# Kernel optimization log

Hardware: AMD Instinct MI355X
Metric: run time of the kernel (lower is better)

## Reference

```python
import math
import jax, jax.numpy as jnp
import numpy as np

EPS = 1e-12
INV_4PI = 1.0 / (4.0 * math.pi)
B, NF = 32768, 3
RES_THETA, RES_PHI = 21, 41


def _make_quadrature(res_theta, res_phi):
    theta = np.linspace(0.0, math.pi, res_theta, dtype=np.float32)
    phi = np.linspace(0.0, 2.0 * math.pi, res_phi, dtype=np.float32)
    tm = 0.5 * (theta[:-1] + theta[1:])
    pm = 0.5 * (phi[:-1] + phi[1:])
    dth = theta[1:] - theta[:-1]
    dph = phi[1:] - phi[:-1]
    st, ct = np.sin(tm), np.cos(tm)
    sp, cp = np.sin(pm), np.cos(pm)
    vx = np.outer(st, cp).reshape(-1)
    vy = np.outer(st, sp).reshape(-1)
    vz = np.outer(ct, np.ones_like(pm)).reshape(-1)
    w = np.outer(st * dth, dph).reshape(-1)
    return (jnp.asarray(vx), jnp.asarray(vy), jnp.asarray(vz), jnp.asarray(w))


def setup_inputs() -> dict:
    key = jax.random.key(0)
    k1, k2, k3 = jax.random.split(key, 3)
    # positive densities O(1), flux magnitude <= 0.9*N (physically valid moments)
    dens = jax.random.uniform(k1, (B, 2, NF), minval=0.3, maxval=1.0, dtype=jnp.float32)
    fdir = jax.random.normal(k2, (B, 2, NF, 3), dtype=jnp.float32)
    fdir = fdir / jnp.clip(jnp.linalg.norm(fdir, axis=-1, keepdims=True), 1e-6)
    fmag = jax.random.uniform(k3, (B, 2, NF), minval=0.0, maxval=0.9, dtype=jnp.float32)
    F = fdir * (dens * fmag)[..., None]
    F4_in = jnp.concatenate([F, dens[..., None]], axis=-1)  # [B,2,NF,4]
    dir_x, dir_y, dir_z, quad_w = _make_quadrature(RES_THETA, RES_PHI)
    return {"F4_in": F4_in, "dir_x": dir_x, "dir_y": dir_y, "dir_z": dir_z, "quad_w": quad_w}


def _z_approxbis(f):
    f = jnp.clip(f, 0.0, 0.999999)
    f2 = f * f
    f4 = f2 * f2
    f6 = f4 * f2
    f8 = f4 * f4
    denom = 3.0 - 1.00651 * f2 - 0.962251 * f4 + 1.47353 * f6 - 0.48953 * f8
    p = 1.0 - 2.0 * (1.0 - f) * (1.0 + 1.01524 * f) / jnp.clip(denom, EPS)
    return 2.0 * f / jnp.clip(1.0 - p, 1e-06)


def _z_over_sinh_z(z):
    small = jnp.abs(z) < 1e-4
    zs = jnp.where(small, 1.0, z)  # avoid 0/0 in unused branch
    series = 1.0 - z * z / 6.0 + (z * z) * (z * z) / 120.0
    return jnp.where(small, series, zs / jnp.sinh(zs))


def _forward(F4_in, dir_x, dir_y, dir_z, quad_w):
    nf = F4_in.shape[2]
    N_e, N_ebar = F4_in[:, 0, 0, 3], F4_in[:, 1, 0, 3]
    F_e, F_ebar = F4_in[:, 0, 0, :3], F4_in[:, 1, 0, :3]
    if nf > 1:
        N_x = jnp.mean(F4_in[:, 0, 1:, 3], axis=1)
        N_xbar = jnp.mean(F4_in[:, 1, 1:, 3], axis=1)
        F_x = jnp.mean(F4_in[:, 0, 1:, :3], axis=1)
        F_xbar = jnp.mean(F4_in[:, 1, 1:, :3], axis=1)
    else:
        N_x, N_xbar, F_x, F_xbar = N_e, N_ebar, F_e, F_ebar
    N = jnp.clip(jnp.stack([N_e, N_ebar, N_x, N_xbar], axis=1), EPS)  # [B,4]
    F = jnp.stack([F_e, F_ebar, F_x, F_xbar], axis=1)  # [B,4,3]
    normF = jnp.sqrt(jnp.sum(F * F, axis=2))  # [B,4]
    fluxfac = jnp.clip(normF / N, 0.0, 0.999999)
    Z = _z_approxbis(fluxfac)  # [B,4]
    # mu: projection of unit direction onto flux direction, [B,4,D]
    mu = (F[:, :, 0, None] * dir_x + F[:, :, 1, None] * dir_y + F[:, :, 2, None] * dir_z) / jnp.clip(normF[..., None], EPS)
    g = N[..., None] * INV_4PI * _z_over_sinh_z(Z)[..., None] * jnp.exp(Z[..., None] * mu)  # [B,4,D]
    gnue, gnuebar, gnux, gnuxbar = g[:, 0], g[:, 1], g[:, 2], g[:, 3]
    delta = gnue - gnuebar - gnux + gnuxbar  # [B,D]
    Hpos = (delta >= 0.0).astype(g.dtype)
    Hneg = 1.0 - Hpos
    Iplus = jnp.sum(quad_w * jnp.maximum(delta, 0.0), axis=1)  # [B]
    Iminus = jnp.sum(quad_w * jnp.maximum(-delta, 0.0), axis=1)
    Ip_s = jnp.clip(Iplus, EPS)
    Im_s = jnp.clip(Iminus, EPS)
    third = jnp.full_like(Iplus, 1.0 / 3.0)
    coeff_pos = jnp.clip(jnp.where(Iplus < Iminus, third, 1.0 - 2.0 / 3.0 * (Im_s / Ip_s)), 0.0, 1.0)
    coeff_neg = jnp.clip(jnp.where(Iplus < Iminus, 1.0 - 2.0 / 3.0 * (Ip_s / Im_s), third), 0.0, 1.0)
    Psur = coeff_pos[:, None] * Hpos + coeff_neg[:, None] * Hneg  # [B,D]
    gnue_t = gnue * Psur + gnux * (1.0 - Psur)
    gnuebar_t = gnuebar * Psur + gnuxbar * (1.0 - Psur)
    gnux_t = 0.5 * (1.0 - Psur) * gnue + 0.5 * (1.0 + Psur) * gnux
    gnuxbar_t = 0.5 * (1.0 - Psur) * gnuebar + 0.5 * (1.0 + Psur) * gnuxbar
    g_t = jnp.stack([gnue_t, gnuebar_t, gnux_t, gnuxbar_t], axis=1)  # [B,4,D]
    gw = g_t * quad_w  # [B,4,D]
    newN = jnp.sum(gw, axis=2)  # [B,4]
    newF = jnp.stack([jnp.sum(gw * dir_x, axis=2), jnp.sum(gw * dir_y, axis=2), jnp.sum(gw * dir_z, axis=2)], axis=2)  # [B,4,3]
    b = F4_in.shape[0]
    if nf > 1:
        F_nu = jnp.concatenate([newF[:, 0:1], jnp.broadcast_to(newF[:, 2:3], (b, nf - 1, 3))], axis=1)
        F_nubar = jnp.concatenate([newF[:, 1:2], jnp.broadcast_to(newF[:, 3:4], (b, nf - 1, 3))], axis=1)
        N_nu = jnp.concatenate([newN[:, 0:1], jnp.broadcast_to(newN[:, 2:3], (b, nf - 1))], axis=1)
        N_nubar = jnp.concatenate([newN[:, 1:2], jnp.broadcast_to(newN[:, 3:4], (b, nf - 1))], axis=1)
    else:
        F_nu, F_nubar = newF[:, 0:1], newF[:, 1:2]
        N_nu, N_nubar = newN[:, 0:1], newN[:, 1:2]
    nu = jnp.concatenate([F_nu, N_nu[..., None]], axis=-1)  # [B,NF,4]
    nubar = jnp.concatenate([F_nubar, N_nubar[..., None]], axis=-1)
    F4mix = jnp.stack([nu, nubar], axis=1)  # [B,2,NF,4]
    growth = jnp.sqrt(jnp.clip(Iplus * Iminus, 0.0))
    return (F4mix, growth)


def reference(F4_in, dir_x, dir_y, dir_z, quad_w):
    return _forward(F4_in, dir_x, dir_y, dir_z, quad_w)
```

## Files before the change

kernel.cpp:

```cpp
#include <hip/hip_runtime.h>
#include <math.h>

#define EPSF     1e-12f
#define INV_4PI  0.07957747154594767f
#define LOG2E    1.4426950408889634f

typedef float v2f __attribute__((ext_vector_type(2)));

#if __has_builtin(__builtin_elementwise_fma)
#define FMA2(a, b, c) __builtin_elementwise_fma((a), (b), (c))
#else
#define FMA2(a, b, c) ((a) * (b) + (c))
#endif

#define EXP2(x) __builtin_amdgcn_exp2f(x)

__device__ __forceinline__ float zapprox(float f) {
    float f2 = f * f;
    float f4 = f2 * f2;
    float f6 = f4 * f2;
    float f8 = f4 * f4;
    float denom = 3.0f - 1.00651f * f2 - 0.962251f * f4 + 1.47353f * f6 - 0.48953f * f8;
    denom = fmaxf(denom, EPSF);
    float p = 1.0f - 2.0f * (1.0f - f) * (1.0f + 1.01524f * f) / denom;
    return 2.0f * f / fmaxf(1.0f - p, 1e-6f);
}

__device__ __forceinline__ float z_over_sinh(float z) {
    float zz = z * z;
    float series = 1.0f - zz / 6.0f + zz * zz / 120.0f;
    float E = __expf(z);
    float s = 0.5f * (E - 1.0f / E);
    float r = z / s;
    return (z < 1e-4f) ? series : r;
}

__device__ __forceinline__ float4 setup_spec(float N, float Fx, float Fy, float Fz) {
    N = fmaxf(N, EPSF);
    float nf = sqrtf(Fx * Fx + Fy * Fy + Fz * Fz);
    float f  = fminf(fmaxf(nf / N, 0.0f), 0.999999f);
    float Z  = zapprox(f);
    float A  = N * INV_4PI * z_over_sinh(Z);
    float sc = Z * LOG2E / fmaxf(nf, EPSF);
    return make_float4(Fx * sc, Fy * sc, Fz * sc, log2f(A));
}

__global__ __launch_bounds__(256) void spec_kernel(
    const float* __restrict__ F4, float4* __restrict__ ws, int B)
{
    int t = blockIdx.x * blockDim.x + threadIdx.x;
    if (t >= 4 * B) return;
    int b = t >> 2, s = t & 3;
    const float4* row = (const float4*)(F4 + (size_t)b * 24);
    float N, Fx, Fy, Fz;
    if (s == 0) {
        float4 a = row[0];  N = a.w; Fx = a.x; Fy = a.y; Fz = a.z;
    } else if (s == 1) {
        float4 a = row[3];  N = a.w; Fx = a.x; Fy = a.y; Fz = a.z;
    } else if (s == 2) {
        float4 a = row[1], c = row[2];
        N = 0.5f * (a.w + c.w); Fx = 0.5f * (a.x + c.x);
        Fy = 0.5f * (a.y + c.y); Fz = 0.5f * (a.z + c.z);
    } else {
        float4 a = row[4], c = row[5];
        N = 0.5f * (a.w + c.w); Fx = 0.5f * (a.x + c.x);
        Fy = 0.5f * (a.y + c.y); Fz = 0.5f * (a.z + c.z);
    }
    ws[(size_t)b * 4 + s] = setup_spec(N, Fx, Fy, Fz);
}

__device__ __forceinline__ v2f bcast(float x) { v2f r; r.x = x; r.y = x; return r; }

__global__ __launch_bounds__(256, 4) void box3d_kernel(
    const float4* __restrict__ ws,
    const float* __restrict__ dxp, const float* __restrict__ dyp,
    const float* __restrict__ dzp, const float* __restrict__ qwp,
    float* __restrict__ out, int B, int ndir)
{
    __shared__ float4 sAB[400], sCD[400];
    const int npair = ndir >> 1;
    for (int p = threadIdx.x; p < npair; p += blockDim.x) {
        int d0 = 2 * p;
        sAB[p] = make_float4(dxp[d0], dxp[d0 + 1], dyp[d0], dyp[d0 + 1]);
        sCD[p] = make_float4(dzp[d0], dzp[d0 + 1], qwp[d0], qwp[d0 + 1]);
    }
    __syncthreads();

    const int sub = threadIdx.x & 15;
    const int b = blockIdx.x * 16 + (threadIdx.x >> 4);
    if (b >= B) return;

    const float4* wsb = ws + (size_t)b * 4;
    float4 f0 = wsb[0], f1 = wsb[1], f2 = wsb[2], f3 = wsb[3];
    v2f zx0 = bcast(f0.x), zy0 = bcast(f0.y), zz0 = bcast(f0.z), la0 = bcast(f0.w);
    v2f zx1 = bcast(f1.x), zy1 = bcast(f1.y), zz1 = bcast(f1.z), la1 = bcast(f1.w);
    v2f zx2 = bcast(f2.x), zy2 = bcast(f2.y), zz2 = bcast(f2.z), la2 = bcast(f2.w);
    v2f zx3 = bcast(f3.x), zy3 = bcast(f3.y), zz3 = bcast(f3.z), la3 = bcast(f3.w);

    const v2f zero = bcast(0.0f);
    v2f aut0 = zero, aut1 = zero, aut2 = zero, aut3 = zero;
    v2f aup0 = zero, aup1 = zero, aup2 = zero, aup3 = zero;
    v2f avt0 = zero, avt1 = zero, avt2 = zero, avt3 = zero;
    v2f avp0 = zero, avp1 = zero, avp2 = zero, avp3 = zero;
    v2f agx0 = zero, agx1 = zero, agx2 = zero, agx3 = zero;
    v2f agy0 = zero, agy1 = zero, agy2 = zero, agy3 = zero;

    #pragma clang loop unroll(disable)
    for (int p = sub; p < npair; p += 16) {
        float4 ab = sAB[p];
        float4 cd = sCD[p];
        v2f qx; qx.x = ab.x; qx.y = ab.y;
        v2f qy; qy.x = ab.z; qy.y = ab.w;
        v2f qz; qz.x = cd.x; qz.y = cd.y;
        v2f qw; qw.x = cd.z; qw.y = cd.w;

        v2f t0 = FMA2(zx0, qx, FMA2(zy0, qy, FMA2(zz0, qz, la0)));
        v2f t1 = FMA2(zx1, qx, FMA2(zy1, qy, FMA2(zz1, qz, la1)));
        v2f t2 = FMA2(zx2, qx, FMA2(zy2, qy, FMA2(zz2, qz, la2)));
        v2f t3 = FMA2(zx3, qx, FMA2(zy3, qy, FMA2(zz3, qz, la3)));
        v2f g0, g1, g2, g3;
        g0.x = EXP2(t0.x); g0.y = EXP2(t0.y);
        g1.x = EXP2(t1.x); g1.y = EXP2(t1.y);
        g2.x = EXP2(t2.x); g2.y = EXP2(t2.y);
        g3.x = EXP2(t3.x); g3.y = EXP2(t3.y);

        v2f u = g0 - g2, v = g1 - g3;
        v2f wu = qw * u, wv = qw * v;
        v2f wup, wvp;
        wup.x = (u.x >= v.x) ? wu.x : 0.0f;
        wup.y = (u.y >= v.y) ? wu.y : 0.0f;
        wvp.x = (u.x >= v.x) ? wv.x : 0.0f;
        wvp.y = (u.y >= v.y) ? wv.y : 0.0f;
        v2f w2 = qw * g2, w3 = qw * g3;

        aut0 += wu;  aup0 += wup;  avt0 += wv;  avp0 += wvp;  agx0 += w2;  agy0 += w3;
        aut1 = FMA2(wu, qx, aut1);  aup1 = FMA2(wup, qx, aup1);
        avt1 = FMA2(wv, qx, avt1);  avp1 = FMA2(wvp, qx, avp1);
        agx1 = FMA2(w2, qx, agx1);  agy1 = FMA2(w3, qx, agy1);
        aut2 = FMA2(wu, qy, aut2);  aup2 = FMA2(wup, qy, aup2);
        avt2 = FMA2(wv, qy, avt2);  avp2 = FMA2(wvp, qy, avp2);
        agx2 = FMA2(w2, qy, agx2);  agy2 = FMA2(w3, qy, agy2);
        aut3 = FMA2(wu, qz, aut3);  aup3 = FMA2(wup, qz, aup3);
        avt3 = FMA2(wv, qz, avt3);  avp3 = FMA2(wvp, qz, avp3);
        agx3 = FMA2(w2, qz, agx3);  agy3 = FMA2(w3, qz, agy3);
    }

    float ut0 = aut0.x + aut0.y, ut1 = aut1.x + aut1.y, ut2 = aut2.x + aut2.y, ut3 = aut3.x + aut3.y;
    float up0 = aup0.x + aup0.y, up1 = aup1.x + aup1.y, up2 = aup2.x + aup2.y, up3 = aup3.x + aup3.y;
    float vt0 = avt0.x + avt0.y, vt1 = avt1.x + avt1.y, vt2 = avt2.x + avt2.y, vt3 = avt3.x + avt3.y;
    float vp0 = avp0.x + avp0.y, vp1 = avp1.x + avp1.y, vp2 = avp2.x + avp2.y, vp3 = avp3.x + avp3.y;
    float gx0 = agx0.x + agx0.y, gx1 = agx1.x + agx1.y, gx2 = agx2.x + agx2.y, gx3 = agx3.x + agx3.y;
    float gy0 = agy0.x + agy0.y, gy1 = agy1.x + agy1.y, gy2 = agy2.x + agy2.y, gy3 = agy3.x + agy3.y;

    #pragma unroll
    for (int msk = 1; msk <= 8; msk <<= 1) {
        ut0 += __shfl_xor(ut0, msk);  ut1 += __shfl_xor(ut1, msk);
        ut2 += __shfl_xor(ut2, msk);  ut3 += __shfl_xor(ut3, msk);
        up0 += __shfl_xor(up0, msk);  up1 += __shfl_xor(up1, msk);
        up2 += __shfl_xor(up2, msk);  up3 += __shfl_xor(up3, msk);
        vt0 += __shfl_xor(vt0, msk);  vt1 += __shfl_xor(vt1, msk);
        vt2 += __shfl_xor(vt2, msk);  vt3 += __shfl_xor(vt3, msk);
        vp0 += __shfl_xor(vp0, msk);  vp1 += __shfl_xor(vp1, msk);
        vp2 += __shfl_xor(vp2, msk);  vp3 += __shfl_xor(vp3, msk);
        gx0 += __shfl_xor(gx0, msk);  gx1 += __shfl_xor(gx1, msk);
        gx2 += __shfl_xor(gx2, msk);  gx3 += __shfl_xor(gx3, msk);
        gy0 += __shfl_xor(gy0, msk);  gy1 += __shfl_xor(gy1, msk);
        gy2 += __shfl_xor(gy2, msk);  gy3 += __shfl_xor(gy3, msk);
    }

    float ip = fmaxf(up0 - vp0, 0.0f);
    float im = fmaxf(ip - ut0 + vt0, 0.0f);

    float Ips = fmaxf(ip, EPSF), Ims = fmaxf(im, EPSF);
    const float third = 1.0f / 3.0f;
    float cp, cn;
    if (ip < im) {
        cp = third;
        cn = fminf(fmaxf(1.0f - (2.0f / 3.0f) * (Ips / Ims), 0.0f), 1.0f);
    } else {
        cp = fminf(fmaxf(1.0f - (2.0f / 3.0f) * (Ims / Ips), 0.0f), 1.0f);
        cn = third;
    }

    float P0 = cp * up0 + cn * (ut0 - up0), Q0 = cp * vp0 + cn * (vt0 - vp0);
    float P1 = cp * up1 + cn * (ut1 - up1), Q1 = cp * vp1 + cn * (vt1 - vp1);
    float P2 = cp * up2 + cn * (ut2 - up2), Q2 = cp * vp2 + cn * (vt2 - vp2);
    float P3 = cp * up3 + cn * (ut3 - up3), Q3 = cp * vp3 + cn * (vt3 - vp3);

    float4* o4 = (float4*)out + (size_t)b * 6;
    if (sub == 0) {
        o4[0] = make_float4(gx1 + P1, gx2 + P2, gx3 + P3, gx0 + P0);
    } else if (sub == 1) {
        o4[1] = make_float4(gx1 + 0.5f * (ut1 - P1), gx2 + 0.5f * (ut2 - P2),
                            gx3 + 0.5f * (ut3 - P3), gx0 + 0.5f * (ut0 - P0));
    } else if (sub == 2) {
        o4[2] = make_float4(gx1 + 0.5f * (ut1 - P1), gx2 + 0.5f * (ut2 - P2),
                            gx3 + 0.5f * (ut3 - P3), gx0 + 0.5f * (ut0 - P0));
    } else if (sub == 3) {
        o4[3] = make_float4(gy1 + Q1, gy2 + Q2, gy3 + Q3, gy0 + Q0);
    } else if (sub == 4) {
        o4[4] = make_float4(gy1 + 0.5f * (vt1 - Q1), gy2 + 0.5f * (vt2 - Q2),
                            gy3 + 0.5f * (vt3 - Q3), gy0 + 0.5f * (vt0 - Q0));
    } else if (sub == 5) {
        o4[5] = make_float4(gy1 + 0.5f * (vt1 - Q1), gy2 + 0.5f * (vt2 - Q2),
                            gy3 + 0.5f * (vt3 - Q3), gy0 + 0.5f * (vt0 - Q0));
    } else if (sub == 6) {
        out[(size_t)B * 24 + b] = sqrtf(fmaxf(ip * im, 0.0f));
    }
}

extern "C" void kernel_launch(void* const* d_in, const int* in_sizes, int n_in,
                              void* d_out, int out_size, void* d_ws, size_t ws_size,
                              hipStream_t stream) {
    const float* F4 = (const float*)d_in[0];
    const float* dx = (const float*)d_in[1];
    const float* dy = (const float*)d_in[2];
    const float* dz = (const float*)d_in[3];
    const float* qw = (const float*)d_in[4];
    float* out = (float*)d_out;

    int B = in_sizes[0] / 24;
    int ndir = in_sizes[1];
    float4* ws = (float4*)d_ws;

    int t1 = 4 * B;
    spec_kernel<<<(t1 + 255) / 256, 256, 0, stream>>>(F4, ws, B);
    int blocks = (B + 15) / 16;
    box3d_kernel<<<blocks, 256, 0, stream>>>(ws, dx, dy, dz, qw, out, B, ndir);
}
```

Baseline: 96.80 us.

## Exploit antipodal quadrature symmetry and fold weights into exponent

Processes only half of the quadrature directions and derives each mirror direction's exponent as 2*(lambda+log2 w) - t. Sums and differences of the paired values then feed the moment accumulators directly. The quadrature weight is folded into the exponent as log2(w), and the hardware exp2 is replaced by a packed polynomial with ldexp. The thread mapping moves to 8 lanes per batch element and 32 elements per block. This relies on the direction grid being antipodally symmetric with mirror points in the second half, and adds polynomial ALU cost in place of the transcendental unit.

Result: slower. 99.27 us (+2.6%).

```diff
diff --git a/kernel.cpp b/kernel.cpp
--- a/kernel.cpp
+++ b/kernel.cpp
@@ -13,7 +13,22 @@
 #define FMA2(a, b, c) ((a) * (b) + (c))
 #endif
 
-#define EXP2(x) __builtin_amdgcn_exp2f(x)
+__device__ __forceinline__ v2f bcast(float x) { v2f r; r.x = x; r.y = x; return r; }
+
+__device__ __forceinline__ v2f exp2p(v2f x) {
+    v2f n; n.x = __builtin_rintf(x.x); n.y = __builtin_rintf(x.y);
+    v2f r = x - n;
+    const v2f c1 = bcast(0.69314718056f);
+    const v2f c2 = bcast(0.24022650700f);
+    const v2f c3 = bcast(0.05550410866f);
+    const v2f c4 = bcast(0.00961812911f);
+    const v2f c5 = bcast(0.00133335581f);
+    v2f p = FMA2(FMA2(FMA2(FMA2(FMA2(c5, r, c4), r, c3), r, c2), r, c1), r, bcast(1.0f));
+    v2f o;
+    o.x = ldexpf(p.x, (int)n.x);
+    o.y = ldexpf(p.y, (int)n.y);
+    return o;
+}
 
 __device__ __forceinline__ float zapprox(float f) {
     float f2 = f * f;
@@ -69,25 +84,23 @@
     ws[(size_t)b * 4 + s] = setup_spec(N, Fx, Fy, Fz);
 }
 
-__device__ __forceinline__ v2f bcast(float x) { v2f r; r.x = x; r.y = x; return r; }
-
 __global__ __launch_bounds__(256, 4) void box3d_kernel(
     const float4* __restrict__ ws,
     const float* __restrict__ dxp, const float* __restrict__ dyp,
     const float* __restrict__ dzp, const float* __restrict__ qwp,
     float* __restrict__ out, int B, int ndir)
 {
-    __shared__ float4 sAB[400], sCD[400];
-    const int npair = ndir >> 1;
-    for (int p = threadIdx.x; p < npair; p += blockDim.x) {
-        int d0 = 2 * p;
-        sAB[p] = make_float4(dxp[d0], dxp[d0 + 1], dyp[d0], dyp[d0 + 1]);
-        sCD[p] = make_float4(dzp[d0], dzp[d0 + 1], qwp[d0], qwp[d0 + 1]);
+    __shared__ float4 sAB[200], sCD[200];
+    const int npp = ndir >> 2;
+    for (int m = threadIdx.x; m < npp; m += blockDim.x) {
+        int d0 = 2 * m, d1 = d0 + 1;
+        sAB[m] = make_float4(dxp[d0], dxp[d1], dyp[d0], dyp[d1]);
+        sCD[m] = make_float4(dzp[d0], dzp[d1], __log2f(qwp[d0]), __log2f(qwp[d1]));
     }
     __syncthreads();
 
-    const int sub = threadIdx.x & 15;
-    const int b = blockIdx.x * 16 + (threadIdx.x >> 4);
+    const int sub = threadIdx.x & 7;
+    const int b = blockIdx.x * 32 + (threadIdx.x >> 3);
     if (b >= B) return;
 
     const float4* wsb = ws + (size_t)b * 4;
@@ -98,6 +111,7 @@
     v2f zx3 = bcast(f3.x), zy3 = bcast(f3.y), zz3 = bcast(f3.z), la3 = bcast(f3.w);
 
     const v2f zero = bcast(0.0f);
+    const v2f two  = bcast(2.0f);
     v2f aut0 = zero, aut1 = zero, aut2 = zero, aut3 = zero;
     v2f aup0 = zero, aup1 = zero, aup2 = zero, aup3 = zero;
     v2f avt0 = zero, avt1 = zero, avt2 = zero, avt3 = zero;
@@ -106,43 +120,49 @@
     v2f agy0 = zero, agy1 = zero, agy2 = zero, agy3 = zero;
 
     #pragma clang loop unroll(disable)
-    for (int p = sub; p < npair; p += 16) {
-        float4 ab = sAB[p];
-        float4 cd = sCD[p];
+    for (int m = sub; m < npp; m += 8) {
+        float4 ab = sAB[m];
+        float4 cd = sCD[m];
         v2f qx; qx.x = ab.x; qx.y = ab.y;
         v2f qy; qy.x = ab.z; qy.y = ab.w;
         v2f qz; qz.x = cd.x; qz.y = cd.y;
-        v2f qw; qw.x = cd.z; qw.y = cd.w;
-
-        v2f t0 = FMA2(zx0, qx, FMA2(zy0, qy, FMA2(zz0, qz, la0)));
-        v2f t1 = FMA2(zx1, qx, FMA2(zy1, qy, FMA2(zz1, qz, la1)));
-        v2f t2 = FMA2(zx2, qx, FMA2(zy2, qy, FMA2(zz2, qz, la2)));
-        v2f t3 = FMA2(zx3, qx, FMA2(zy3, qy, FMA2(zz3, qz, la3)));
-        v2f g0, g1, g2, g3;
-        g0.x = EXP2(t0.x); g0.y = EXP2(t0.y);
-        g1.x = EXP2(t1.x); g1.y = EXP2(t1.y);
-        g2.x = EXP2(t2.x); g2.y = EXP2(t2.y);
-        g3.x = EXP2(t3.x); g3.y = EXP2(t3.y);
-
-        v2f u = g0 - g2, v = g1 - g3;
-        v2f wu = qw * u, wv = qw * v;
-        v2f wup, wvp;
-        wup.x = (u.x >= v.x) ? wu.x : 0.0f;
-        wup.y = (u.y >= v.y) ? wu.y : 0.0f;
-        wvp.x = (u.x >= v.x) ? wv.x : 0.0f;
-        wvp.y = (u.y >= v.y) ? wv.y : 0.0f;
-        v2f w2 = qw * g2, w3 = qw * g3;
-
-        aut0 += wu;  aup0 += wup;  avt0 += wv;  avp0 += wvp;  agx0 += w2;  agy0 += w3;
-        aut1 = FMA2(wu, qx, aut1);  aup1 = FMA2(wup, qx, aup1);
-        avt1 = FMA2(wv, qx, avt1);  avp1 = FMA2(wvp, qx, avp1);
-        agx1 = FMA2(w2, qx, agx1);  agy1 = FMA2(w3, qx, agy1);
-        aut2 = FMA2(wu, qy, aut2);  aup2 = FMA2(wup, qy, aup2);
-        avt2 = FMA2(wv, qy, avt2);  avp2 = FMA2(wvp, qy, avp2);
-        agx2 = FMA2(w2, qy, agx2);  agy2 = FMA2(w3, qy, agy2);
-        aut3 = FMA2(wu, qz, aut3);  aup3 = FMA2(wup, qz, aup3);
-        avt3 = FMA2(wv, qz, avt3);  avp3 = FMA2(wvp, qz, avp3);
-        agx3 = FMA2(w2, qz, agx3);  agy3 = FMA2(w3, qz, agy3);
+        v2f lw; lw.x = cd.z; lw.y = cd.w;
+
+        v2f b0 = la0 + lw, b1 = la1 + lw, b2 = la2 + lw, b3 = la3 + lw;
+        v2f t0 = FMA2(zx0, qx, FMA2(zy0, qy, FMA2(zz0, qz, b0)));
+        v2f t1 = FMA2(zx1, qx, FMA2(zy1, qy, FMA2(zz1, qz, b1)));
+        v2f t2 = FMA2(zx2, qx, FMA2(zy2, qy, FMA2(zz2, qz, b2)));
+        v2f t3 = FMA2(zx3, qx, FMA2(zy3, qy, FMA2(zz3, qz, b3)));
+        v2f n0 = FMA2(two, b0, -t0);
+        v2f n1 = FMA2(two, b1, -t1);
+        v2f n2 = FMA2(two, b2, -t2);
+        v2f n3 = FMA2(two, b3, -t3);
+
+        v2f gp0 = exp2p(t0), gp1 = exp2p(t1), gp2 = exp2p(t2), gp3 = exp2p(t3);
+        v2f gn0 = exp2p(n0), gn1 = exp2p(n1), gn2 = exp2p(n2), gn3 = exp2p(n3);
+
+        v2f uP = gp0 - gp2, vP = gp1 - gp3;
+        v2f uN = gn0 - gn2, vN = gn1 - gn3;
+
+        v2f suP, svP, suN, svN;
+        suP.x = (uP.x >= vP.x) ? uP.x : 0.0f;  suP.y = (uP.y >= vP.y) ? uP.y : 0.0f;
+        svP.x = (uP.x >= vP.x) ? vP.x : 0.0f;  svP.y = (uP.y >= vP.y) ? vP.y : 0.0f;
+        suN.x = (uN.x >= vN.x) ? uN.x : 0.0f;  suN.y = (uN.y >= vN.y) ? uN.y : 0.0f;
+        svN.x = (uN.x >= vN.x) ? vN.x : 0.0f;  svN.y = (uN.y >= vN.y) ? vN.y : 0.0f;
+
+        v2f s, d;
+        s = uP + uN;   d = uP - uN;
+        aut0 += s; aut1 = FMA2(d, qx, aut1); aut2 = FMA2(d, qy, aut2); aut3 = FMA2(d, qz, aut3);
+        s = suP + suN; d = suP - suN;
+        aup0 += s; aup1 = FMA2(d, qx, aup1); aup2 = FMA2(d, qy, aup2); aup3 = FMA2(d, qz, aup3);
+        s = vP + vN;   d = vP - vN;
+        avt0 += s; avt1 = FMA2(d, qx, avt1); avt2 = FMA2(d, qy, avt2); avt3 = FMA2(d, qz, avt3);
+        s = svP + svN; d = svP - svN;
+        avp0 += s; avp1 = FMA2(d, qx, avp1); avp2 = FMA2(d, qy, avp2); avp3 = FMA2(d, qz, avp3);
+        s = gp2 + gn2; d = gp2 - gn2;
+        agx0 += s; agx1 = FMA2(d, qx, agx1); agx2 = FMA2(d, qy, agx2); agx3 = FMA2(d, qz, agx3);
+        s = gp3 + gn3; d = gp3 - gn3;
+        agy0 += s; agy1 = FMA2(d, qx, agy1); agy2 = FMA2(d, qy, agy2); agy3 = FMA2(d, qz, agy3);
     }
 
     float ut0 = aut0.x + aut0.y, ut1 = aut1.x + aut1.y, ut2 = aut2.x + aut2.y, ut3 = aut3.x + aut3.y;
@@ -153,7 +173,7 @@
     float gy0 = agy0.x + agy0.y, gy1 = agy1.x + agy1.y, gy2 = agy2.x + agy2.y, gy3 = agy3.x + agy3.y;
 
     #pragma unroll
-    for (int msk = 1; msk <= 8; msk <<= 1) {
+    for (int msk = 1; msk <= 4; msk <<= 1) {
         ut0 += __shfl_xor(ut0, msk);  ut1 += __shfl_xor(ut1, msk);
         ut2 += __shfl_xor(ut2, msk);  ut3 += __shfl_xor(ut3, msk);
         up0 += __shfl_xor(up0, msk);  up1 += __shfl_xor(up1, msk);
@@ -225,6 +245,6 @@
 
     int t1 = 4 * B;
     spec_kernel<<<(t1 + 255) / 256, 256, 0, stream>>>(F4, ws, B);
-    int blocks = (B + 15) / 16;
+    int blocks = (B + 31) / 32;
     box3d_kernel<<<blocks, 256, 0, stream>>>(ws, dx, dy, dz, qw, out, B, ndir);
 }
```

## Exploit antipodal quadrature symmetry and restructure box3d as lane-per-batch with LDS reduction

Applied to the files above, without the earlier changes.

Each lane now owns one batch element, and the 16 waves of a 1024-thread block split the first half of the directions. For each direction the kernel also evaluates the antipodal direction by reusing the exponent algebraically (2*lambda - t) and negating the direction in the moment accumulation. This halves direction loads and dot-product work and turns direction reads into wave-uniform loads. The per-batch cross-lane shuffle reduction is replaced by a two-stage LDS reduction across waves, and all six outputs are written by one lane. It relies on the quadrature being antipodally symmetric with equal weights, which holds for this construction but is not checked. It also adds several block-wide barriers and uses a large block.

Result: faster. 92.06 us (-4.9%).

```diff
diff --git a/kernel.cpp b/kernel.cpp
--- a/kernel.cpp
+++ b/kernel.cpp
@@ -14,6 +14,8 @@
 #endif
 
 #define EXP2(x) __builtin_amdgcn_exp2f(x)
+
+__device__ __forceinline__ v2f bcast(float x) { v2f r; r.x = x; r.y = x; return r; }
 
 __device__ __forceinline__ float zapprox(float f) {
     float f2 = f * f;
@@ -69,104 +71,147 @@
     ws[(size_t)b * 4 + s] = setup_spec(N, Fx, Fy, Fz);
 }
 
-__device__ __forceinline__ v2f bcast(float x) { v2f r; r.x = x; r.y = x; return r; }
-
-__global__ __launch_bounds__(256, 4) void box3d_kernel(
+__device__ __forceinline__ void add4(float4& a, const float4 b) {
+    a.x += b.x; a.y += b.y; a.z += b.z; a.w += b.w;
+}
+
+__global__ __launch_bounds__(1024, 8) void box3d_kernel(
     const float4* __restrict__ ws,
     const float* __restrict__ dxp, const float* __restrict__ dyp,
     const float* __restrict__ dzp, const float* __restrict__ qwp,
     float* __restrict__ out, int B, int ndir)
 {
-    __shared__ float4 sAB[400], sCD[400];
-    const int npair = ndir >> 1;
-    for (int p = threadIdx.x; p < npair; p += blockDim.x) {
-        int d0 = 2 * p;
-        sAB[p] = make_float4(dxp[d0], dxp[d0 + 1], dyp[d0], dyp[d0 + 1]);
-        sCD[p] = make_float4(dzp[d0], dzp[d0 + 1], qwp[d0], qwp[d0 + 1]);
-    }
-    __syncthreads();
-
-    const int sub = threadIdx.x & 15;
-    const int b = blockIdx.x * 16 + (threadIdx.x >> 4);
-    if (b >= B) return;
-
-    const float4* wsb = ws + (size_t)b * 4;
-    float4 f0 = wsb[0], f1 = wsb[1], f2 = wsb[2], f3 = wsb[3];
-    v2f zx0 = bcast(f0.x), zy0 = bcast(f0.y), zz0 = bcast(f0.z), la0 = bcast(f0.w);
-    v2f zx1 = bcast(f1.x), zy1 = bcast(f1.y), zz1 = bcast(f1.z), la1 = bcast(f1.w);
-    v2f zx2 = bcast(f2.x), zy2 = bcast(f2.y), zz2 = bcast(f2.z), la2 = bcast(f2.w);
-    v2f zx3 = bcast(f3.x), zy3 = bcast(f3.y), zz3 = bcast(f3.z), la3 = bcast(f3.w);
+    __shared__ float4 red[16][64][3];
+
+    const int lane = threadIdx.x & 63;
+    const int w    = __builtin_amdgcn_readfirstlane(threadIdx.x >> 6);
+    const int b    = blockIdx.x * 64 + lane;
+    const bool live = (b < B);
+
+    v2f zx01, zy01, zz01, la01, zx23, zy23, zz23, la23;
+    if (live) {
+        const float4* wsb = ws + (size_t)b * 4;
+        float4 s0 = wsb[0], s1 = wsb[1], s2 = wsb[2], s3 = wsb[3];
+        zx01.x = s0.x; zx01.y = s1.x;  zx23.x = s2.x; zx23.y = s3.x;
+        zy01.x = s0.y; zy01.y = s1.y;  zy23.x = s2.y; zy23.y = s3.y;
+        zz01.x = s0.z; zz01.y = s1.z;  zz23.x = s2.z; zz23.y = s3.z;
+        la01.x = s0.w; la01.y = s1.w;  la23.x = s2.w; la23.y = s3.w;
+    } else {
+        zx01 = zy01 = zz01 = la01 = bcast(0.0f);
+        zx23 = zy23 = zz23 = la23 = bcast(0.0f);
+    }
+    const v2f two = bcast(2.0f);
+
+    const int nst   = ndir >> 1;
+    const int chunk = (nst + 15) >> 4;
+    const int d0    = w * chunk;
+    const int d1    = (d0 + chunk < nst) ? d0 + chunk : nst;
 
     const v2f zero = bcast(0.0f);
-    v2f aut0 = zero, aut1 = zero, aut2 = zero, aut3 = zero;
-    v2f aup0 = zero, aup1 = zero, aup2 = zero, aup3 = zero;
-    v2f avt0 = zero, avt1 = zero, avt2 = zero, avt3 = zero;
-    v2f avp0 = zero, avp1 = zero, avp2 = zero, avp3 = zero;
-    v2f agx0 = zero, agx1 = zero, agx2 = zero, agx3 = zero;
-    v2f agy0 = zero, agy1 = zero, agy2 = zero, agy3 = zero;
+    v2f auv0 = zero, auv1 = zero, auv2 = zero, auv3 = zero;
+    v2f asv0 = zero, asv1 = zero, asv2 = zero, asv3 = zero;
+    v2f ag0  = zero, ag1  = zero, ag2  = zero, ag3  = zero;
+
+    int dd = (d0 < d1) ? d0 : 0;
+    float qx = dxp[dd], qy = dyp[dd], qz = dzp[dd], qw = qwp[dd];
 
     #pragma clang loop unroll(disable)
-    for (int p = sub; p < npair; p += 16) {
-        float4 ab = sAB[p];
-        float4 cd = sCD[p];
-        v2f qx; qx.x = ab.x; qx.y = ab.y;
-        v2f qy; qy.x = ab.z; qy.y = ab.w;
-        v2f qz; qz.x = cd.x; qz.y = cd.y;
-        v2f qw; qw.x = cd.z; qw.y = cd.w;
-
-        v2f t0 = FMA2(zx0, qx, FMA2(zy0, qy, FMA2(zz0, qz, la0)));
-        v2f t1 = FMA2(zx1, qx, FMA2(zy1, qy, FMA2(zz1, qz, la1)));
-        v2f t2 = FMA2(zx2, qx, FMA2(zy2, qy, FMA2(zz2, qz, la2)));
-        v2f t3 = FMA2(zx3, qx, FMA2(zy3, qy, FMA2(zz3, qz, la3)));
-        v2f g0, g1, g2, g3;
-        g0.x = EXP2(t0.x); g0.y = EXP2(t0.y);
-        g1.x = EXP2(t1.x); g1.y = EXP2(t1.y);
-        g2.x = EXP2(t2.x); g2.y = EXP2(t2.y);
-        g3.x = EXP2(t3.x); g3.y = EXP2(t3.y);
-
-        v2f u = g0 - g2, v = g1 - g3;
-        v2f wu = qw * u, wv = qw * v;
-        v2f wup, wvp;
-        wup.x = (u.x >= v.x) ? wu.x : 0.0f;
-        wup.y = (u.y >= v.y) ? wu.y : 0.0f;
-        wvp.x = (u.x >= v.x) ? wv.x : 0.0f;
-        wvp.y = (u.y >= v.y) ? wv.y : 0.0f;
-        v2f w2 = qw * g2, w3 = qw * g3;
-
-        aut0 += wu;  aup0 += wup;  avt0 += wv;  avp0 += wvp;  agx0 += w2;  agy0 += w3;
-        aut1 = FMA2(wu, qx, aut1);  aup1 = FMA2(wup, qx, aup1);
-        avt1 = FMA2(wv, qx, avt1);  avp1 = FMA2(wvp, qx, avp1);
-        agx1 = FMA2(w2, qx, agx1);  agy1 = FMA2(w3, qx, agy1);
-        aut2 = FMA2(wu, qy, aut2);  aup2 = FMA2(wup, qy, aup2);
-        avt2 = FMA2(wv, qy, avt2);  avp2 = FMA2(wvp, qy, avp2);
-        agx2 = FMA2(w2, qy, agx2);  agy2 = FMA2(w3, qy, agy2);
-        aut3 = FMA2(wu, qz, aut3);  aup3 = FMA2(wup, qz, aup3);
-        avt3 = FMA2(wv, qz, avt3);  avp3 = FMA2(wvp, qz, avp3);
-        agx3 = FMA2(w2, qz, agx3);  agy3 = FMA2(w3, qz, agy3);
-    }
-
-    float ut0 = aut0.x + aut0.y, ut1 = aut1.x + aut1.y, ut2 = aut2.x + aut2.y, ut3 = aut3.x + aut3.y;
-    float up0 = aup0.x + aup0.y, up1 = aup1.x + aup1.y, up2 = aup2.x + aup2.y, up3 = aup3.x + aup3.y;
-    float vt0 = avt0.x + avt0.y, vt1 = avt1.x + avt1.y, vt2 = avt2.x + avt2.y, vt3 = avt3.x + avt3.y;
-    float vp0 = avp0.x + avp0.y, vp1 = avp1.x + avp1.y, vp2 = avp2.x + avp2.y, vp3 = avp3.x + avp3.y;
-    float gx0 = agx0.x + agx0.y, gx1 = agx1.x + agx1.y, gx2 = agx2.x + agx2.y, gx3 = agx3.x + agx3.y;
-    float gy0 = agy0.x + agy0.y, gy1 = agy1.x + agy1.y, gy2 = agy2.x + agy2.y, gy3 = agy3.x + agy3.y;
-
+    for (int d = d0; d < d1; ++d) {
+        int dn = (d + 1 < d1) ? d + 1 : d;
+        float nqx = dxp[dn], nqy = dyp[dn], nqz = dzp[dn], nqw = qwp[dn];
+
+        v2f t01 = FMA2(zx01, bcast(qx), FMA2(zy01, bcast(qy), FMA2(zz01, bcast(qz), la01)));
+        v2f t23 = FMA2(zx23, bcast(qx), FMA2(zy23, bcast(qy), FMA2(zz23, bcast(qz), la23)));
+
+        {
+            v2f g01, g23;
+            g01.x = EXP2(t01.x); g01.y = EXP2(t01.y);
+            g23.x = EXP2(t23.x); g23.y = EXP2(t23.y);
+            v2f uv = bcast(qw) * (g01 - g23);
+            v2f wg = bcast(qw) * g23;
+            bool c = (uv.x >= uv.y);
+            v2f suv; suv.x = c ? uv.x : 0.0f; suv.y = c ? uv.y : 0.0f;
+            auv0 += uv;  auv1 = FMA2(uv, bcast(qx), auv1);
+            auv2 = FMA2(uv, bcast(qy), auv2);  auv3 = FMA2(uv, bcast(qz), auv3);
+            asv0 += suv; asv1 = FMA2(suv, bcast(qx), asv1);
+            asv2 = FMA2(suv, bcast(qy), asv2); asv3 = FMA2(suv, bcast(qz), asv3);
+            ag0  += wg;  ag1  = FMA2(wg, bcast(qx), ag1);
+            ag2  = FMA2(wg, bcast(qy), ag2);   ag3  = FMA2(wg, bcast(qz), ag3);
+        }
+        {
+            v2f n01 = FMA2(two, la01, -t01);
+            v2f n23 = FMA2(two, la23, -t23);
+            v2f g01, g23;
+            g01.x = EXP2(n01.x); g01.y = EXP2(n01.y);
+            g23.x = EXP2(n23.x); g23.y = EXP2(n23.y);
+            v2f uv = bcast(qw) * (g01 - g23);
+            v2f wg = bcast(qw) * g23;
+            bool c = (uv.x >= uv.y);
+            v2f suv; suv.x = c ? uv.x : 0.0f; suv.y = c ? uv.y : 0.0f;
+            auv0 += uv;  auv1 = FMA2(uv, bcast(-qx), auv1);
+            auv2 = FMA2(uv, bcast(-qy), auv2);  auv3 = FMA2(uv, bcast(-qz), auv3);
+            asv0 += suv; asv1 = FMA2(suv, bcast(-qx), asv1);
+            asv2 = FMA2(suv, bcast(-qy), asv2); asv3 = FMA2(suv, bcast(-qz), asv3);
+            ag0  += wg;  ag1  = FMA2(wg, bcast(-qx), ag1);
+            ag2  = FMA2(wg, bcast(-qy), ag2);   ag3  = FMA2(wg, bcast(-qz), ag3);
+        }
+        qx = nqx; qy = nqy; qz = nqz; qw = nqw;
+    }
+
+    float4 rA0 = make_float4(auv0.x, auv0.y, auv1.x, auv1.y);
+    float4 rA1 = make_float4(auv2.x, auv2.y, auv3.x, auv3.y);
+    float4 rA2 = make_float4(asv0.x, asv0.y, asv1.x, asv1.y);
+    float4 rB0 = make_float4(asv2.x, asv2.y, asv3.x, asv3.y);
+    float4 rB1 = make_float4(ag0.x,  ag0.y,  ag1.x,  ag1.y);
+    float4 rB2 = make_float4(ag2.x,  ag2.y,  ag3.x,  ag3.y);
+
+    red[w][lane][0] = rA0; red[w][lane][1] = rA1; red[w][lane][2] = rA2;
+    __syncthreads();
+    if (w < 4) {
+        #pragma unroll
+        for (int o = 4; o < 16; o += 4) {
+            add4(rA0, red[w + o][lane][0]);
+            add4(rA1, red[w + o][lane][1]);
+            add4(rA2, red[w + o][lane][2]);
+        }
+        red[w][lane][0] = rA0; red[w][lane][1] = rA1; red[w][lane][2] = rA2;
+    }
+    __syncthreads();
+    if (w == 0) {
+        #pragma unroll
+        for (int o = 1; o < 4; ++o) {
+            add4(rA0, red[o][lane][0]);
+            add4(rA1, red[o][lane][1]);
+            add4(rA2, red[o][lane][2]);
+        }
+    }
+    __syncthreads();
+    red[w][lane][0] = rB0; red[w][lane][1] = rB1; red[w][lane][2] = rB2;
+    __syncthreads();
+    if (w < 4) {
+        #pragma unroll
+        for (int o = 4; o < 16; o += 4) {
+            add4(rB0, red[w + o][lane][0]);
+            add4(rB1, red[w + o][lane][1]);
+            add4(rB2, red[w + o][lane][2]);
+        }
+        red[w][lane][0] = rB0; red[w][lane][1] = rB1; red[w][lane][2] = rB2;
+    }
+    __syncthreads();
+    if (w != 0 || !live) return;
     #pragma unroll
-    for (int msk = 1; msk <= 8; msk <<= 1) {
-        ut0 += __shfl_xor(ut0, msk);  ut1 += __shfl_xor(ut1, msk);
-        ut2 += __shfl_xor(ut2, msk);  ut3 += __shfl_xor(ut3, msk);
-        up0 += __shfl_xor(up0, msk);  up1 += __shfl_xor(up1, msk);
-        up2 += __shfl_xor(up2, msk);  up3 += __shfl_xor(up3, msk);
-        vt0 += __shfl_xor(vt0, msk);  vt1 += __shfl_xor(vt1, msk);
-        vt2 += __shfl_xor(vt2, msk);  vt3 += __shfl_xor(vt3, msk);
-        vp0 += __shfl_xor(vp0, msk);  vp1 += __shfl_xor(vp1, msk);
-        vp2 += __shfl_xor(vp2, msk);  vp3 += __shfl_xor(vp3, msk);
-        gx0 += __shfl_xor(gx0, msk);  gx1 += __shfl_xor(gx1, msk);
-        gx2 += __shfl_xor(gx2, msk);  gx3 += __shfl_xor(gx3, msk);
-        gy0 += __shfl_xor(gy0, msk);  gy1 += __shfl_xor(gy1, msk);
-        gy2 += __shfl_xor(gy2, msk);  gy3 += __shfl_xor(gy3, msk);
-    }
+    for (int o = 1; o < 4; ++o) {
+        add4(rB0, red[o][lane][0]);
+        add4(rB1, red[o][lane][1]);
+        add4(rB2, red[o][lane][2]);
+    }
+
+    float ut0 = rA0.x, vt0 = rA0.y, ut1 = rA0.z, vt1 = rA0.w;
+    float ut2 = rA1.x, vt2 = rA1.y, ut3 = rA1.z, vt3 = rA1.w;
+    float up0 = rA2.x, vp0 = rA2.y, up1 = rA2.z, vp1 = rA2.w;
+    float up2 = rB0.x, vp2 = rB0.y, up3 = rB0.z, vp3 = rB0.w;
+    float gx0 = rB1.x, gy0 = rB1.y, gx1 = rB1.z, gy1 = rB1.w;
+    float gx2 = rB2.x, gy2 = rB2.y, gx3 = rB2.z, gy3 = rB2.w;
 
     float ip = fmaxf(up0 - vp0, 0.0f);
     float im = fmaxf(ip - ut0 + vt0, 0.0f);
@@ -188,25 +233,15 @@
     float P3 = cp * up3 + cn * (ut3 - up3), Q3 = cp * vp3 + cn * (vt3 - vp3);
 
     float4* o4 = (float4*)out + (size_t)b * 6;
-    if (sub == 0) {
-        o4[0] = make_float4(gx1 + P1, gx2 + P2, gx3 + P3, gx0 + P0);
-    } else if (sub == 1) {
-        o4[1] = make_float4(gx1 + 0.5f * (ut1 - P1), gx2 + 0.5f * (ut2 - P2),
+    float4 oe = make_float4(gx1 + P1, gx2 + P2, gx3 + P3, gx0 + P0);
+    float4 ox = make_float4(gx1 + 0.5f * (ut1 - P1), gx2 + 0.5f * (ut2 - P2),
                             gx3 + 0.5f * (ut3 - P3), gx0 + 0.5f * (ut0 - P0));
-    } else if (sub == 2) {
-        o4[2] = make_float4(gx1 + 0.5f * (ut1 - P1), gx2 + 0.5f * (ut2 - P2),
-                            gx3 + 0.5f * (ut3 - P3), gx0 + 0.5f * (ut0 - P0));
-    } else if (sub == 3) {
-        o4[3] = make_float4(gy1 + Q1, gy2 + Q2, gy3 + Q3, gy0 + Q0);
-    } else if (sub == 4) {
-        o4[4] = make_float4(gy1 + 0.5f * (vt1 - Q1), gy2 + 0.5f * (vt2 - Q2),
-                            gy3 + 0.5f * (vt3 - Q3), gy0 + 0.5f * (vt0 - Q0));
-    } else if (sub == 5) {
-        o4[5] = make_float4(gy1 + 0.5f * (vt1 - Q1), gy2 + 0.5f * (vt2 - Q2),
-                            gy3 + 0.5f * (vt3 - Q3), gy0 + 0.5f * (vt0 - Q0));
-    } else if (sub == 6) {
-        out[(size_t)B * 24 + b] = sqrtf(fmaxf(ip * im, 0.0f));
-    }
+    float4 ob = make_float4(gy1 + Q1, gy2 + Q2, gy3 + Q3, gy0 + Q0);
+    float4 oxb = make_float4(gy1 + 0.5f * (vt1 - Q1), gy2 + 0.5f * (vt2 - Q2),
+                             gy3 + 0.5f * (vt3 - Q3), gy0 + 0.5f * (vt0 - Q0));
+    o4[0] = oe;  o4[1] = ox;  o4[2] = ox;
+    o4[3] = ob;  o4[4] = oxb; o4[5] = oxb;
+    out[(size_t)B * 24 + b] = sqrtf(fmaxf(ip * im, 0.0f));
 }
 
 extern "C" void kernel_launch(void* const* d_in, const int* in_sizes, int n_in,
@@ -225,6 +260,6 @@
 
     int t1 = 4 * B;
     spec_kernel<<<(t1 + 255) / 256, 256, 0, stream>>>(F4, ws, B);
-    int blocks = (B + 15) / 16;
-    box3d_kernel<<<blocks, 256, 0, stream>>>(ws, dx, dy, dz, qw, out, B, ndir);
-}
+    int blocks = (B + 63) / 64;
+    box3d_kernel<<<blocks, 1024, 0, stream>>>(ws, dx, dy, dz, qw, out, B, ndir);
+}
```
